# Performance work log

Measured on AMD Instinct MI355X. Metric: run time of the kernel, lower is better.

The kernel has to match this reference:

```python
import jax, jax.numpy as jnp
import numpy as np

K_CHAINS, N_STATES, ALPHABET, SEQ_LEN = 3, 12, 32, 64


def setup_inputs() -> dict:
    key = jax.random.key(0)
    k0, k1, k2, k3, k4 = jax.random.split(key, 5)
    return {
        "ys": jax.random.randint(k0, (SEQ_LEN,), 0, ALPHABET),
        "transition": jax.random.normal(k1, (K_CHAINS, N_STATES, N_STATES), jnp.float32),
        "emission": jax.random.normal(k2, (K_CHAINS, N_STATES, ALPHABET), jnp.float32),
        "choice": jax.random.normal(k3, (K_CHAINS,), jnp.float32),
        "prior": jax.random.normal(k4, (K_CHAINS, N_STATES), jnp.float32),
    }


def reference(ys, transition, emission, choice, prior):
    K, S = transition.shape[0], transition.shape[1]
    c = jax.nn.log_softmax(choice)                  # (K,)
    t = jax.nn.log_softmax(transition, axis=-1)     # (K,S,S)
    e = jax.nn.log_softmax(emission, axis=-1)       # (K,S,A)
    p = jax.nn.log_softmax(prior, axis=-1)          # (K,S)

    # enumerate expanded state space: tuples (s_1..s_K, i) -> N = S^K * K rows
    grids = jnp.meshgrid(*([jnp.arange(S)] * K + [jnp.arange(K)]), indexing="ij")
    tbl = jnp.stack(grids, -1).reshape(-1, K + 1)   # (N, K+1)
    states = tbl[:, :K]                             # (N, K) chain states
    chain = tbl[:, K]                               # (N,)   active chain index

    # transition matrix A[m, n] = logprob(old expanded state n -> new expanded state m)
    onehot = jax.nn.one_hot(chain, K, dtype=bool)   # (N, K)
    eq = states[:, None, :] == states[None, :, :]   # (N_new, N_old, K)
    valid = jnp.where(onehot[:, None, :], True, eq).all(-1)  # non-active chains unchanged
    s_new = jnp.take_along_axis(states, chain[:, None], axis=1)[:, 0]  # (N,) new state of active chain
    s_old = states[:, chain]                        # (N_old, N_new): old state at chain[m]
    t_term = t[chain[None, :], s_old, s_new[None, :]]  # (N_old, N_new)
    Amat = c[chain][:, None] + t_term.T + jnp.where(valid, 0.0, -jnp.inf)  # (N_new, N_old)

    # emission table B[m, y] = e[chain[m], state of active chain, y]
    B = e[chain, s_new]                             # (N, A)

    # initial alpha: sum_j p[j, s_j] + c[i]
    alpha0 = p[jnp.arange(K)[None, :], states].sum(-1) + c[chain]  # (N,)

    def step(alpha, y):
        alpha = B[:, y] + jax.nn.logsumexp(alpha[None, :] + Amat, axis=-1)
        return alpha, None

    alpha, _ = jax.lax.scan(step, alpha0, ys)
    return jax.nn.logsumexp(alpha)
```

## Files before the change

kernel.cpp:

```cpp
#include <hip/hip_runtime.h>
#include <math.h>

#define KC 3
#define S 12
#define SS 1728
#define AB 32
#define TLEN 64
#define NTHREADS 448
#define NWAVES 7
#define NSLICE 432
#define LN2F 0.69314718055994530942f

__device__ __forceinline__ int swz_word(int n) {
    int r   = n / 12;
    int pos = n % 12;
    int v = (((r & 1) << 2) | (pos >> 2)) ^ ((r >> 1) & 7);
    return ((r >> 1) << 5) + (v << 2) + (pos & 3);
}

__global__ __launch_bounds__(NTHREADS, 2)
void hmm_fwd_kernel(const int* __restrict__ ys,
                    const float* __restrict__ transition,
                    const float* __restrict__ emission,
                    const float* __restrict__ choice,
                    const float* __restrict__ prior,
                    float* __restrict__ out)
{
    __shared__ __align__(16) float ABUF[5760];
    __shared__ __align__(16) float BETA[2304];
    __shared__ __align__(16) float ECt[KC*AB*S];
    __shared__ float T_s[KC][S][S];
    __shared__ float p_lin[KC][S];
    __shared__ float c_lin[KC];
    __shared__ int   ys_s[TLEN];
    __shared__ float wsum[NWAVES];

    const int tid = threadIdx.x;

    if (tid < TLEN) ys_s[tid] = ys[tid];

    if (tid == 0) {
        float m = fmaxf(fmaxf(choice[0], choice[1]), choice[2]);
        float e0 = __expf(choice[0]-m), e1 = __expf(choice[1]-m), e2 = __expf(choice[2]-m);
        float inv = 1.f / (e0+e1+e2);
        c_lin[0] = e0*inv; c_lin[1] = e1*inv; c_lin[2] = e2*inv;
    }
    if (tid >= 1 && tid < 1 + KC) {
        int k = tid - 1;
        float m = -INFINITY;
        #pragma unroll
        for (int i = 0; i < S; ++i) m = fmaxf(m, prior[k*S + i]);
        float ev[S]; float s = 0.f;
        #pragma unroll
        for (int i = 0; i < S; ++i) { ev[i] = __expf(prior[k*S + i] - m); s += ev[i]; }
        float inv = 1.f / s;
        #pragma unroll
        for (int i = 0; i < S; ++i) p_lin[k][i] = ev[i] * inv;
    }
    if (tid >= 64 && tid < 64 + KC*S) {
        int r = tid - 64;
        int k = r / S, i = r % S;
        const float* row = transition + (k*S + i)*S;
        float m = -INFINITY;
        #pragma unroll
        for (int j = 0; j < S; ++j) m = fmaxf(m, row[j]);
        float ev[S]; float s = 0.f;
        #pragma unroll
        for (int j = 0; j < S; ++j) { ev[j] = __expf(row[j] - m); s += ev[j]; }
        float inv = 1.f / s;
        #pragma unroll
        for (int j = 0; j < S; ++j) T_s[k][i][j] = ev[j] * inv;
    }
    if (tid >= 128 && tid < 128 + KC*S) {
        int r = tid - 128;
        int k = r / S, sj = r % S;
        float cm = fmaxf(fmaxf(choice[0], choice[1]), choice[2]);
        float ce = __expf(choice[k]-cm) /
                   (__expf(choice[0]-cm) + __expf(choice[1]-cm) + __expf(choice[2]-cm));
        const float* row = emission + (k*S + sj)*AB;
        float m = -INFINITY;
        #pragma unroll
        for (int a = 0; a < AB; ++a) m = fmaxf(m, row[a]);
        float ev[AB]; float s = 0.f;
        #pragma unroll
        for (int a = 0; a < AB; ++a) { ev[a] = __expf(row[a] - m); s += ev[a]; }
        float inv = ce / s;
        #pragma unroll
        for (int a = 0; a < AB; ++a) ECt[(k*AB + a)*S + sj] = ev[a] * inv;
    }
    __syncthreads();

    const bool active = tid < NSLICE;
    const int sk = tid / 144;
    const int q  = tid % 144;

    int rd[S], wr[S];
    float4 T4[S][3];

    if (active) {
        int n[S];
        if (sk == 0) {
            #pragma unroll
            for (int j = 0; j < S; ++j) n[j] = j*144 + q;
        } else if (sk == 1) {
            int b = (q/12)*144 + (q%12);
            #pragma unroll
            for (int j = 0; j < S; ++j) n[j] = b + j*12;
        } else {
            #pragma unroll
            for (int j = 0; j < S; ++j) n[j] = q*12 + j;
        }
        #pragma unroll
        for (int j = 0; j < S; ++j) rd[j] = swz_word(n[j]);
        #pragma unroll
        for (int j = 0; j < S; ++j)
            wr[j] = (sk == 0) ? n[j] : (sk == 1 ? 1728 + n[j] : 3456 + swz_word(n[j]));

        #pragma unroll
        for (int i = 0; i < S; ++i) {
            #pragma unroll
            for (int c = 0; c < 3; ++c) {
                T4[i][c] = *reinterpret_cast<const float4*>(&T_s[sk][i][4*c]);
                asm volatile("" : "+v"(T4[i][c].x), "+v"(T4[i][c].y),
                                  "+v"(T4[i][c].z), "+v"(T4[i][c].w));
            }
        }

        float pq = (sk == 0) ? p_lin[1][q/12] * p_lin[2][q%12]
                 : (sk == 1) ? p_lin[0][q/12] * p_lin[2][q%12]
                 :             p_lin[0][q/12] * p_lin[1][q%12];
        float ck = c_lin[sk];
        #pragma unroll
        for (int j = 0; j < S; ++j) ABUF[wr[j]] = p_lin[sk][j] * pq * ck;
    }
    const int p13 = tid / 3, pm3 = tid % 3;
    const int swzw = ((p13 >> 1) << 5) + ((((((p13 & 1) << 2) | pm3)) ^ ((p13 >> 1) & 7)) << 2);
    __syncthreads();

    float logR = 0.f, invR = 1.f;

    for (int t = 0; t < TLEN; ++t) {
        const int y = ys_s[t];
        float4 b4, e0, e1, e2;

        if (active) {
            float4 a0 = *reinterpret_cast<const float4*>(&ABUF[4*tid]);
            float4 a1 = *reinterpret_cast<const float4*>(&ABUF[1728 + 4*tid]);
            float4 a2 = *reinterpret_cast<const float4*>(&ABUF[3456 + swzw]);
            b4.x = a0.x + a1.x + a2.x;
            b4.y = a0.y + a1.y + a2.y;
            b4.z = a0.z + a1.z + a2.z;
            b4.w = a0.w + a1.w + a2.w;
            *reinterpret_cast<float4*>(&BETA[swzw]) = b4;
            const float* eb = &ECt[(sk*AB + y)*S];
            e0 = *reinterpret_cast<const float4*>(&eb[0]);
            e1 = *reinterpret_cast<const float4*>(&eb[4]);
            e2 = *reinterpret_cast<const float4*>(&eb[8]);
        }
        __syncthreads();

        float4 o0, o1, o2;
        if (active) {
            float bv[S];
            #pragma unroll
            for (int i = 0; i < S; ++i) bv[i] = BETA[rd[i]];

            float4 acc0 = {0,0,0,0}, acc1 = {0,0,0,0}, acc2 = {0,0,0,0};
            #pragma unroll
            for (int i = 0; i < S; ++i) {
                const float b = bv[i];
                acc0.x += b*T4[i][0].x; acc0.y += b*T4[i][0].y;
                acc0.z += b*T4[i][0].z; acc0.w += b*T4[i][0].w;
                acc1.x += b*T4[i][1].x; acc1.y += b*T4[i][1].y;
                acc1.z += b*T4[i][1].z; acc1.w += b*T4[i][1].w;
                acc2.x += b*T4[i][2].x; acc2.y += b*T4[i][2].y;
                acc2.z += b*T4[i][2].z; acc2.w += b*T4[i][2].w;
            }
            o0.x = acc0.x*e0.x*invR; o0.y = acc0.y*e0.y*invR;
            o0.z = acc0.z*e0.z*invR; o0.w = acc0.w*e0.w*invR;
            o1.x = acc1.x*e1.x*invR; o1.y = acc1.y*e1.y*invR;
            o1.z = acc1.z*e1.z*invR; o1.w = acc1.w*e1.w*invR;
            o2.x = acc2.x*e2.x*invR; o2.y = acc2.y*e2.y*invR;
            o2.z = acc2.z*e2.z*invR; o2.w = acc2.w*e2.w*invR;

            ABUF[wr[0]]  = o0.x; ABUF[wr[1]]  = o0.y; ABUF[wr[2]]  = o0.z; ABUF[wr[3]]  = o0.w;
            ABUF[wr[4]]  = o1.x; ABUF[wr[5]]  = o1.y; ABUF[wr[6]]  = o1.z; ABUF[wr[7]]  = o1.w;
            ABUF[wr[8]]  = o2.x; ABUF[wr[9]]  = o2.y; ABUF[wr[10]] = o2.z; ABUF[wr[11]] = o2.w;
        }

        if ((t & 7) == 7) {
            float part = 0.f;
            if (active) {
                part = (o0.x+o0.y+o0.z+o0.w) + (o1.x+o1.y+o1.z+o1.w) + (o2.x+o2.y+o2.z+o2.w);
            }
            #pragma unroll
            for (int o = 32; o > 0; o >>= 1) part += __shfl_xor(part, o);
            if ((tid & 63) == 0) wsum[tid >> 6] = part;
        }
        __syncthreads();

        if ((t & 7) == 7 && t < TLEN-1) {
            float R = wsum[0];
            #pragma unroll
            for (int w = 1; w < NWAVES; ++w) R += wsum[w];
            invR = __builtin_amdgcn_rcpf(R);
            logR += __log2f(R);
        } else {
            invR = 1.f;
        }
    }

    if (tid == 0) {
        float R = wsum[0];
        #pragma unroll
        for (int w = 1; w < NWAVES; ++w) R += wsum[w];
        out[0] = LN2F * (__log2f(R) + logR);
    }
}

extern "C" void kernel_launch(void* const* d_in, const int* in_sizes, int n_in,
                              void* d_out, int out_size, void* d_ws, size_t ws_size,
                              hipStream_t stream) {
    const int*   ys         = (const int*)  d_in[0];
    const float* transition = (const float*)d_in[1];
    const float* emission   = (const float*)d_in[2];
    const float* choice     = (const float*)d_in[3];
    const float* prior      = (const float*)d_in[4];
    float* out = (float*)d_out;

    hipLaunchKernelGGL(hmm_fwd_kernel, dim3(1), dim3(NTHREADS), 0, stream,
                       ys, transition, emission, choice, prior, out);
}
```

Baseline: 65.46 us.

## Replace swizzled shared buffers with stride-13 padded per-chain layouts

Replaces the XOR-swizzled shared alpha/beta buffers with three per-chain alpha arrays and three beta copies, each padded to a row stride of 13. Every thread can then read and write one contiguous row with conflict-free scalar accesses instead of precomputed index tables. The rescale factor moves from the output stage into the beta summation, and the transition matrix is held as scalar registers. The cost is three shared-memory writes of each beta value per step, plus scalar rather than vector LDS accesses.

```diff
diff --git a/kernel.cpp b/kernel.cpp
--- a/kernel.cpp
+++ b/kernel.cpp
@@ -9,14 +9,8 @@
 #define NTHREADS 448
 #define NWAVES 7
 #define NSLICE 432
+#define ROWW 13
 #define LN2F 0.69314718055994530942f
-
-__device__ __forceinline__ int swz_word(int n) {
-    int r   = n / 12;
-    int pos = n % 12;
-    int v = (((r & 1) << 2) | (pos >> 2)) ^ ((r >> 1) & 7);
-    return ((r >> 1) << 5) + (v << 2) + (pos & 3);
-}
 
 __global__ __launch_bounds__(NTHREADS, 2)
 void hmm_fwd_kernel(const int* __restrict__ ys,
@@ -26,9 +20,9 @@
                     const float* __restrict__ prior,
                     float* __restrict__ out)
 {
-    __shared__ __align__(16) float ABUF[5760];
-    __shared__ __align__(16) float BETA[2304];
-    __shared__ __align__(16) float ECt[KC*AB*S];
+    __shared__ float P0[144*ROWW], P1[144*ROWW], P2[144*ROWW];
+    __shared__ float BR[144*ROWW], BQ[144*ROWW], BP[144*ROWW];
+    __shared__ float ECt[KC*AB*S];
     __shared__ float T_s[KC][S][S];
     __shared__ float p_lin[KC][S];
     __shared__ float c_lin[KC];
@@ -94,107 +88,95 @@
     const int sk = tid / 144;
     const int q  = tid % 144;
 
-    int rd[S], wr[S];
-    float4 T4[S][3];
-
+    const float* rdp = (sk == 0) ? &BR[ROWW*q] : (sk == 1) ? &BQ[ROWW*q] : &BP[ROWW*q];
+    float*       wrp = (sk == 0) ? &P0[ROWW*q] : (sk == 1) ? &P1[ROWW*q] : &P2[ROWW*q];
+    const float* ecb = &ECt[sk*AB*S];
+
+    const int s0f = tid / 36;
+    const int s1f = (4*tid % 144) / 12;
+    const int s2b = (4*tid) % 12;
+    const int bRo = ROWW*(12*s1f + s2b) + s0f;
+    const int bQo = ROWW*(12*s0f + s2b) + s1f;
+    const int bPo = ROWW*(12*s0f + s1f) + s2b;
+
+    float Treg[S][S];
     if (active) {
-        int n[S];
-        if (sk == 0) {
-            #pragma unroll
-            for (int j = 0; j < S; ++j) n[j] = j*144 + q;
-        } else if (sk == 1) {
-            int b = (q/12)*144 + (q%12);
-            #pragma unroll
-            for (int j = 0; j < S; ++j) n[j] = b + j*12;
-        } else {
-            #pragma unroll
-            for (int j = 0; j < S; ++j) n[j] = q*12 + j;
-        }
-        #pragma unroll
-        for (int j = 0; j < S; ++j) rd[j] = swz_word(n[j]);
-        #pragma unroll
-        for (int j = 0; j < S; ++j)
-            wr[j] = (sk == 0) ? n[j] : (sk == 1 ? 1728 + n[j] : 3456 + swz_word(n[j]));
-
         #pragma unroll
         for (int i = 0; i < S; ++i) {
             #pragma unroll
-            for (int c = 0; c < 3; ++c) {
-                T4[i][c] = *reinterpret_cast<const float4*>(&T_s[sk][i][4*c]);
-                asm volatile("" : "+v"(T4[i][c].x), "+v"(T4[i][c].y),
-                                  "+v"(T4[i][c].z), "+v"(T4[i][c].w));
-            }
-        }
-
+            for (int j = 0; j < S; ++j) {
+                float tmp = T_s[sk][i][j];
+                asm volatile("v_mov_b32 %0, %1" : "=v"(Treg[i][j]) : "v"(tmp));
+            }
+        }
         float pq = (sk == 0) ? p_lin[1][q/12] * p_lin[2][q%12]
                  : (sk == 1) ? p_lin[0][q/12] * p_lin[2][q%12]
                  :             p_lin[0][q/12] * p_lin[1][q%12];
         float ck = c_lin[sk];
         #pragma unroll
-        for (int j = 0; j < S; ++j) ABUF[wr[j]] = p_lin[sk][j] * pq * ck;
-    }
-    const int p13 = tid / 3, pm3 = tid % 3;
-    const int swzw = ((p13 >> 1) << 5) + ((((((p13 & 1) << 2) | pm3)) ^ ((p13 >> 1) & 7)) << 2);
+        for (int j = 0; j < S; ++j) wrp[j] = p_lin[sk][j] * pq * ck;
+    }
     __syncthreads();
 
     float logR = 0.f, invR = 1.f;
 
     for (int t = 0; t < TLEN; ++t) {
         const int y = ys_s[t];
-        float4 b4, e0, e1, e2;
 
         if (active) {
-            float4 a0 = *reinterpret_cast<const float4*>(&ABUF[4*tid]);
-            float4 a1 = *reinterpret_cast<const float4*>(&ABUF[1728 + 4*tid]);
-            float4 a2 = *reinterpret_cast<const float4*>(&ABUF[3456 + swzw]);
-            b4.x = a0.x + a1.x + a2.x;
-            b4.y = a0.y + a1.y + a2.y;
-            b4.z = a0.z + a1.z + a2.z;
-            b4.w = a0.w + a1.w + a2.w;
-            *reinterpret_cast<float4*>(&BETA[swzw]) = b4;
-            const float* eb = &ECt[(sk*AB + y)*S];
-            e0 = *reinterpret_cast<const float4*>(&eb[0]);
-            e1 = *reinterpret_cast<const float4*>(&eb[4]);
-            e2 = *reinterpret_cast<const float4*>(&eb[8]);
+            float b[4];
+            #pragma unroll
+            for (int e = 0; e < 4; ++e) {
+                float r = P0[bRo + ROWW*e];
+                float g = P1[bQo + ROWW*e];
+                float h = P2[bPo + e];
+                b[e] = (r + g + h) * invR;
+            }
+            #pragma unroll
+            for (int e = 0; e < 4; ++e) {
+                BR[bRo + ROWW*e] = b[e];
+                BQ[bQo + ROWW*e] = b[e];
+                BP[bPo + e]      = b[e];
+            }
         }
         __syncthreads();
 
-        float4 o0, o1, o2;
+        float o[S];
         if (active) {
+            const float* eb = &ecb[y*S];
+            float4 e0 = *reinterpret_cast<const float4*>(&eb[0]);
+            float4 e1 = *reinterpret_cast<const float4*>(&eb[4]);
+            float4 e2 = *reinterpret_cast<const float4*>(&eb[8]);
+
             float bv[S];
             #pragma unroll
-            for (int i = 0; i < S; ++i) bv[i] = BETA[rd[i]];
-
-            float4 acc0 = {0,0,0,0}, acc1 = {0,0,0,0}, acc2 = {0,0,0,0};
+            for (int i = 0; i < S; ++i) bv[i] = rdp[i];
+
+            float acc[S];
+            #pragma unroll
+            for (int j = 0; j < S; ++j) acc[j] = 0.f;
             #pragma unroll
             for (int i = 0; i < S; ++i) {
-                const float b = bv[i];
-                acc0.x += b*T4[i][0].x; acc0.y += b*T4[i][0].y;
-                acc0.z += b*T4[i][0].z; acc0.w += b*T4[i][0].w;
-                acc1.x += b*T4[i][1].x; acc1.y += b*T4[i][1].y;
-                acc1.z += b*T4[i][1].z; acc1.w += b*T4[i][1].w;
-                acc2.x += b*T4[i][2].x; acc2.y += b*T4[i][2].y;
-                acc2.z += b*T4[i][2].z; acc2.w += b*T4[i][2].w;
-            }
-            o0.x = acc0.x*e0.x*invR; o0.y = acc0.y*e0.y*invR;
-            o0.z = acc0.z*e0.z*invR; o0.w = acc0.w*e0.w*invR;
-            o1.x = acc1.x*e1.x*invR; o1.y = acc1.y*e1.y*invR;
-            o1.z = acc1.z*e1.z*invR; o1.w = acc1.w*e1.w*invR;
-            o2.x = acc2.x*e2.x*invR; o2.y = acc2.y*e2.y*invR;
-            o2.z = acc2.z*e2.z*invR; o2.w = acc2.w*e2.w*invR;
-
-            ABUF[wr[0]]  = o0.x; ABUF[wr[1]]  = o0.y; ABUF[wr[2]]  = o0.z; ABUF[wr[3]]  = o0.w;
-            ABUF[wr[4]]  = o1.x; ABUF[wr[5]]  = o1.y; ABUF[wr[6]]  = o1.z; ABUF[wr[7]]  = o1.w;
-            ABUF[wr[8]]  = o2.x; ABUF[wr[9]]  = o2.y; ABUF[wr[10]] = o2.z; ABUF[wr[11]] = o2.w;
+                const float bb = bv[i];
+                #pragma unroll
+                for (int j = 0; j < S; ++j) acc[j] = __builtin_fmaf(bb, Treg[i][j], acc[j]);
+            }
+            o[0] = acc[0]*e0.x; o[1] = acc[1]*e0.y; o[2]  = acc[2]*e0.z;  o[3]  = acc[3]*e0.w;
+            o[4] = acc[4]*e1.x; o[5] = acc[5]*e1.y; o[6]  = acc[6]*e1.z;  o[7]  = acc[7]*e1.w;
+            o[8] = acc[8]*e2.x; o[9] = acc[9]*e2.y; o[10] = acc[10]*e2.z; o[11] = acc[11]*e2.w;
+
+            #pragma unroll
+            for (int j = 0; j < S; ++j) wrp[j] = o[j];
         }
 
         if ((t & 7) == 7) {
             float part = 0.f;
             if (active) {
-                part = (o0.x+o0.y+o0.z+o0.w) + (o1.x+o1.y+o1.z+o1.w) + (o2.x+o2.y+o2.z+o2.w);
-            }
-            #pragma unroll
-            for (int o = 32; o > 0; o >>= 1) part += __shfl_xor(part, o);
+                #pragma unroll
+                for (int j = 0; j < S; ++j) part += o[j];
+            }
+            #pragma unroll
+            for (int w = 32; w > 0; w >>= 1) part += __shfl_xor(part, w);
             if ((tid & 63) == 0) wsum[tid >> 6] = part;
         }
         __syncthreads();
```

After: 71.25 us. 1.09x slower.
